# Kernel optimization log

Measured on AMD Instinct MI355X. Metric: run time of the kernel, lower is better.

The kernel has to match this reference:

```python
import jax, jax.numpy as jnp
import numpy as np

N = 100000      # nodes
E = 1600000     # edges (avg degree 16)
IN = 128
H = 128
OUT = 112
L = 4           # num GCN2Conv layers per net
NETS = 3        # ensemble size (hardcoded n=3 in module)
ALPHA = 0.1
THETA = 0.5


def setup_inputs() -> dict:
    key = jax.random.key(0)
    ks = jax.random.split(key, 9)
    x = jax.random.normal(ks[0], (N, IN), jnp.float32)
    edge_index = jax.random.randint(ks[1], (2, E), 0, N, dtype=jnp.int32).astype(jnp.int64)
    edge_weight = jax.random.uniform(ks[2], (E,), jnp.float32)
    # nn.Linear default init: U(-1/sqrt(fan_in), 1/sqrt(fan_in))
    s_in = 1.0 / np.sqrt(IN)
    s_h = 1.0 / np.sqrt(H)
    lin0_w = jax.random.uniform(ks[3], (NETS, IN, H), jnp.float32, -s_in, s_in)
    lin0_b = jax.random.uniform(ks[4], (NETS, H), jnp.float32, -s_in, s_in)
    lin1_w = jax.random.uniform(ks[5], (NETS, H, OUT), jnp.float32, -s_h, s_h)
    lin1_b = jax.random.uniform(ks[6], (NETS, OUT), jnp.float32, -s_h, s_h)
    # GCN2Conv shared weight per layer: glorot-ish uniform
    conv_w = jax.random.uniform(ks[7], (NETS, L, H, H), jnp.float32, -s_h, s_h)
    return {"x": x, "edge_index": edge_index, "edge_weight": edge_weight,
            "lin0_w": lin0_w, "lin0_b": lin0_b, "lin1_w": lin1_w,
            "lin1_b": lin1_b, "conv_w": conv_w}


def _net_forward(x, src, dst, ew, w0, b0, w1, b1, cw):
    # x: [N, IN] -> log-probs [N, OUT]; one GCN2 sub-net (eval mode, dropout=0)
    h = jax.nn.relu(x @ w0 + b0)           # [N, H]
    x0 = h
    for l in range(L):
        beta = float(np.log(THETA / (l + 1) + 1.0))
        # sparse propagation: adj_t @ h with 'add' aggregation
        agg = jax.ops.segment_sum(h[src] * ew[:, None], dst, num_segments=N)  # [N, H]
        t = (1.0 - ALPHA) * agg + ALPHA * x0        # initial residual
        h = jax.nn.relu((1.0 - beta) * t + beta * (t @ cw[l]))  # identity mapping
    out = h @ w1 + b1                       # [N, OUT]
    return jax.nn.log_softmax(out, axis=-1)


def reference(x, edge_index, edge_weight, lin0_w, lin0_b, lin1_w, lin1_b, conv_w):
    src, dst = edge_index[0], edge_index[1]
    outs = [
        _net_forward(x, src, dst, edge_weight,
                     lin0_w[n], lin0_b[n], lin1_w[n], lin1_b[n], conv_w[n])
        for n in range(NETS)
    ]
    return jnp.mean(jnp.stack(outs, axis=0), axis=0)  # [N, OUT]
```

## Files before the change

kernel.cpp:

```cpp
#include <hip/hip_runtime.h>
#include <hip/hip_bf16.h>

#define NNODES 100000
#define NEDGES 1600000
#define INF_   128
#define HF     128
#define OUTF   112
#define NLAYERS 4
#define NNETS  3

typedef __attribute__((ext_vector_type(8))) short bf16x8;
typedef __attribute__((ext_vector_type(8))) unsigned short u16x8;
typedef __attribute__((ext_vector_type(4))) float f32x4;
typedef __attribute__((ext_vector_type(2))) unsigned int u32x2;
typedef unsigned long long u64;
typedef unsigned int u32;

__device__ __forceinline__ float bf2f(short u){
  unsigned x = ((unsigned)(unsigned short)u) << 16;
  return __builtin_bit_cast(float, x);
}
__device__ __forceinline__ unsigned short f2bf(float f){
  unsigned u = __builtin_bit_cast(unsigned, f);
  u += 0x7fffu + ((u >> 16) & 1u);
  return (unsigned short)(u >> 16);
}
__device__ __forceinline__ float ub(u32 q, int j){ return (float)((q >> (8*j)) & 0xFF); }


__global__ void detect_fmt(const u64* __restrict__ ei64, int* __restrict__ flag){
  u64 v = ei64[threadIdx.x];
  u64 b = __ballot((v >> 32) != 0ull);
  if (threadIdx.x == 0) flag[0] = (b == 0ull) ? 1 : 0;
}

__device__ __forceinline__ int load_dst(const int* ei, int is64, int e){
  return is64 ? ei[2*(NEDGES + e)] : ei[NEDGES + e];
}
__device__ __forceinline__ int load_src(const int* ei, int is64, int e){
  return is64 ? ei[2*e] : ei[e];
}

__global__ void zero_counts(int* counts){
  int i = blockIdx.x*256 + threadIdx.x;
  if (i < NNODES) counts[i] = 0;
}

__global__ void hist_kernel(const int* __restrict__ ei, const int* __restrict__ flag, int* counts){
  int e = blockIdx.x*256 + threadIdx.x;
  if (e < NEDGES){
    int d = load_dst(ei, flag[0], e);
    if ((unsigned)d < NNODES) atomicAdd(&counts[d], 1);
  }
}

__global__ __launch_bounds__(256) void scan1(const int* __restrict__ counts,
                                             int* __restrict__ scanned,
                                             int* __restrict__ partials){
  __shared__ int s[256];
  int t = threadIdx.x, i = blockIdx.x*256 + t;
  int v = (i < NNODES) ? counts[i] : 0;
  s[t] = v; __syncthreads();
  for (int off=1; off<256; off<<=1){
    int a = (t >= off) ? s[t-off] : 0;
    __syncthreads();
    s[t] += a;
    __syncthreads();
  }
  if (i < NNODES) scanned[i] = s[t] - v;
  if (t == 255) partials[blockIdx.x] = s[255];
}

__global__ __launch_bounds__(512) void scan2(int* partials, int G){
  __shared__ int s[512];
  int t = threadIdx.x;
  int v = (t < G) ? partials[t] : 0;
  s[t] = v; __syncthreads();
  for (int off=1; off<512; off<<=1){
    int a = (t >= off) ? s[t-off] : 0;
    __syncthreads();
    s[t] += a;
    __syncthreads();
  }
  if (t < G) partials[t] = s[t] - v;
}

__global__ void scan3(const int* __restrict__ scanned, const int* __restrict__ partials,
                      int* __restrict__ row_ptr, int* __restrict__ cursor){
  int i = blockIdx.x*256 + threadIdx.x;
  if (i < NNODES){
    int v = scanned[i] + partials[i>>8];
    row_ptr[i] = v;
    cursor[i]  = v;
  } else if (i == NNODES){
    row_ptr[NNODES] = NEDGES;
  }
}

__global__ void scatter_kernel(const int* __restrict__ ei, const float* __restrict__ ew,
                               const int* __restrict__ flag,
                               int* cursor, u32* __restrict__ meta){
  int e = blockIdx.x*256 + threadIdx.x;
  if (e < NEDGES){
    int is64 = flag[0];
    int s = load_src(ei, is64, e);
    int d = load_dst(ei, is64, e);
    float w = __builtin_nontemporal_load(&ew[e]);
    if ((unsigned)d < NNODES && (unsigned)s < NNODES){
      int pos = atomicAdd(&cursor[d], 1);
      if ((unsigned)pos < NEDGES){
        u32 wb = __builtin_bit_cast(u32, w);
        u32 w15 = ((wb + 0x8000u) >> 16) & 0x7FFFu;
        __builtin_nontemporal_store((w15 << 17) | (u32)s, &meta[pos]);
      }
    }
  }
}

__global__ void prep_w(const float* __restrict__ w0, const float* __restrict__ cw,
                       const float* __restrict__ w1,
                       short* __restrict__ w0t, short* __restrict__ cwt, short* __restrict__ w1t){
  int i = blockIdx.x*256 + threadIdx.x;
  const int n0 = NNETS*HF*HF;
  const int n1 = NNETS*NLAYERS*HF*HF;
  const int n2 = NNETS*OUTF*HF;
  if (i < n0){
    int net = i/(HF*HF), r = i%(HF*HF), c = r/HF, k = r%HF;
    w0t[i] = (short)f2bf(w0[(size_t)net*HF*HF + k*HF + c]);
  } else if (i < n0 + n1){
    int j = i - n0;
    int nl = j/(HF*HF), r = j%(HF*HF), c = r/HF, kp = r%HF;
    int k = ((kp&7)<<4) | (kp>>3);
    cwt[j] = (short)f2bf(cw[(size_t)nl*HF*HF + k*HF + c]);
  } else if (i < n0 + n1 + n2){
    int j = i - n0 - n1;
    int net = j/(OUTF*HF), r = j%(OUTF*HF), c = r/HF, kp = r%HF;
    int k = ((kp&7)<<4) | (kp>>3);
    w1t[j] = (short)f2bf(w1[(size_t)net*HF*OUTF + k*OUTF + c]);
  }
}

__global__ __launch_bounds__(256) void gemm_in(
    const float* __restrict__ x, const short* __restrict__ w0t, const float* __restrict__ b0,
    unsigned char* __restrict__ h8, float* __restrict__ sc,
    unsigned char* __restrict__ x08, float* __restrict__ scx)
{
  __shared__ short As[128*128];
  const int t = threadIdx.x;
  const int rowBase = blockIdx.x * 128;
  #pragma unroll
  for (int it=0; it<8; ++it){
    int r = it*16 + (t>>4);
    int k = (t&15)*8;
    int gr = rowBase + r;
    bf16x8 v = {0,0,0,0,0,0,0,0};
    if (gr < NNODES){
      f32x4 f0 = __builtin_nontemporal_load((const f32x4*)&x[(size_t)gr*128 + k]);
      f32x4 f1 = __builtin_nontemporal_load((const f32x4*)&x[(size_t)gr*128 + k + 4]);
      v[0]=(short)f2bf(f0[0]); v[1]=(short)f2bf(f0[1]); v[2]=(short)f2bf(f0[2]); v[3]=(short)f2bf(f0[3]);
      v[4]=(short)f2bf(f1[0]); v[5]=(short)f2bf(f1[1]); v[6]=(short)f2bf(f1[2]); v[7]=(short)f2bf(f1[3]);
    }
    *(bf16x8*)&As[r*128 + (k ^ ((r&7)<<3))] = v;
  }
  __syncthreads();

  const int wid = t>>6, lane = t&63;
  const int l16 = lane&15, kg = lane>>4;
  for (int net=0; net<NNETS; ++net){
    const short* Wt = w0t + (size_t)net*HF*HF;
    f32x4 acc[2][8];
    #pragma unroll
    for (int mt=0; mt<2; ++mt)
      #pragma unroll
      for (int nt=0; nt<8; ++nt){ acc[mt][nt][0]=0.f; acc[mt][nt][1]=0.f; acc[mt][nt][2]=0.f; acc[mt][nt][3]=0.f; }
    #pragma unroll
    for (int ks=0; ks<4; ++ks){
      int k0 = ks*32 + kg*8;
      bf16x8 a0, a1;
      { int r = wid*32 + l16;      a0 = *(const bf16x8*)&As[r*128 + (k0 ^ ((r&7)<<3))]; }
      { int r = wid*32 + 16 + l16; a1 = *(const bf16x8*)&As[r*128 + (k0 ^ ((r&7)<<3))]; }
      #pragma unroll
      for (int nt=0; nt<8; ++nt){
        bf16x8 b = *(const bf16x8*)&Wt[(size_t)(nt*16 + l16)*128 + k0];
        acc[0][nt] = __builtin_amdgcn_mfma_f32_16x16x32_bf16(a0, b, acc[0][nt], 0, 0, 0);
        acc[1][nt] = __builtin_amdgcn_mfma_f32_16x16x32_bf16(a1, b, acc[1][nt], 0, 0, 0);
      }
    }
    #pragma unroll
    for (int mt=0; mt<2; ++mt){
      #pragma unroll
      for (int j=0; j<4; ++j){
        int row = rowBase + wid*32 + mt*16 + kg*4 + j;
        float v[8]; float mx = 0.f;
        #pragma unroll
        for (int nt=0; nt<8; ++nt){
          float f = fmaxf(acc[mt][nt][j] + b0[net*HF + nt*16 + l16], 0.f);
          v[nt] = f; mx = fmaxf(mx, f);
        }
        #pragma unroll
        for (int off=1; off<16; off<<=1) mx = fmaxf(mx, __shfl_xor(mx, off));
        if (row < NNODES){
          float inv = (mx > 0.f) ? 255.f/mx : 0.f;
          u32 d0=0, d1=0;
          #pragma unroll
          for (int nt=0; nt<4; ++nt) d0 |= ((u32)(v[nt]*inv + 0.5f)) << (8*nt);
          #pragma unroll
          for (int nt=0; nt<4; ++nt) d1 |= ((u32)(v[4+nt]*inv + 0.5f)) << (8*nt);
          u32x2 pk; pk[0]=d0; pk[1]=d1;
          size_t off8 = (size_t)row*384 + net*128 + l16*8;
          *(u32x2*)&h8 [off8] = pk;
          *(u32x2*)&x08[off8] = pk;
          if (l16 == 0){ float s = mx * (1.f/255.f); sc[row*4 + net] = s; scx[row*4 + net] = s; }
        }
      }
    }
  }
}

__global__ __launch_bounds__(256) void gemm_mid(
    const unsigned char* __restrict__ agg8, const float* __restrict__ sca,
    const unsigned char* __restrict__ x08,  const float* __restrict__ scx,
    const short* __restrict__ W, const float beta,
    unsigned char* __restrict__ h8, float* __restrict__ sc)
{
  __shared__ short As[128*128];
  const int t = threadIdx.x;
  const int net = blockIdx.y;
  const int rowBase = blockIdx.x * 128;
  const short* Wt = W + (size_t)net*NLAYERS*HF*HF;

  #pragma unroll
  for (int it=0; it<8; ++it){
    int r = it*16 + (t>>4);
    int k = (t&15)*8;
    int gr = rowBase + r;
    bf16x8 v = {0,0,0,0,0,0,0,0};
    if (gr < NNODES){
      size_t off8 = (size_t)gr*384 + net*128 + k;
      u32x2 da = *(const u32x2*)&agg8[off8];
      u32x2 dx = *(const u32x2*)&x08[off8];
      float sa = 0.9f * sca[gr*4 + net];
      float sx = 0.1f * scx[gr*4 + net];
      #pragma unroll
      for (int j=0; j<4; ++j) v[j]   = (short)f2bf(sa*ub(da[0],j) + sx*ub(dx[0],j));
      #pragma unroll
      for (int j=0; j<4; ++j) v[4+j] = (short)f2bf(sa*ub(da[1],j) + sx*ub(dx[1],j));
    }
    *(bf16x8*)&As[r*128 + (k ^ ((r&7)<<3))] = v;
  }
  __syncthreads();

  const int wid = t>>6, lane = t&63;
  const int l16 = lane&15, kg = lane>>4;
  f32x4 acc[2][8];
  #pragma unroll
  for (int mt=0; mt<2; ++mt)
    #pragma unroll
    for (int nt=0; nt<8; ++nt){ acc[mt][nt][0]=0.f; acc[mt][nt][1]=0.f; acc[mt][nt][2]=0.f; acc[mt][nt][3]=0.f; }

  #pragma unroll
  for (int ks=0; ks<4; ++ks){
    int k0 = ks*32 + kg*8;
    bf16x8 a0, a1;
    { int r = wid*32 + l16;      a0 = *(const bf16x8*)&As[r*128 + (k0 ^ ((r&7)<<3))]; }
    { int r = wid*32 + 16 + l16; a1 = *(const bf16x8*)&As[r*128 + (k0 ^ ((r&7)<<3))]; }
    #pragma unroll
    for (int nt=0; nt<8; ++nt){
      bf16x8 b = *(const bf16x8*)&Wt[(size_t)(nt*16 + l16)*128 + k0];
      acc[0][nt] = __builtin_amdgcn_mfma_f32_16x16x32_bf16(a0, b, acc[0][nt], 0, 0, 0);
      acc[1][nt] = __builtin_amdgcn_mfma_f32_16x16x32_bf16(a1, b, acc[1][nt], 0, 0, 0);
    }
  }

  #pragma unroll
  for (int mt=0; mt<2; ++mt){
    #pragma unroll
    for (int j=0; j<4; ++j){
      int rl  = wid*32 + mt*16 + kg*4 + j;
      int row = rowBase + rl;
      float v[8]; float mx = 0.f;
      #pragma unroll
      for (int nt=0; nt<8; ++nt){
        int p = l16*8 + nt;
        float av = bf2f(As[rl*128 + (p ^ ((rl&7)<<3))]);
        float f = fmaxf((1.f-beta)*av + beta*acc[mt][nt][j], 0.f);
        v[nt] = f; mx = fmaxf(mx, f);
      }
      #pragma unroll
      for (int off=1; off<16; off<<=1) mx = fmaxf(mx, __shfl_xor(mx, off));
      if (row < NNODES){
        float inv = (mx > 0.f) ? 255.f/mx : 0.f;
        u32 d0=0, d1=0;
        #pragma unroll
        for (int nt=0; nt<4; ++nt) d0 |= ((u32)(v[nt]*inv + 0.5f)) << (8*nt);
        #pragma unroll
        for (int nt=0; nt<4; ++nt) d1 |= ((u32)(v[4+nt]*inv + 0.5f)) << (8*nt);
        u32x2 pk; pk[0]=d0; pk[1]=d1;
        *(u32x2*)&h8[(size_t)row*384 + net*128 + l16*8] = pk;
        if (l16 == 0) sc[row*4 + net] = mx * (1.f/255.f);
      }
    }
  }
}

__global__ __launch_bounds__(256) void gemm_out(
    const unsigned char* __restrict__ h8, const float* __restrict__ sc,
    const short* __restrict__ w1t, const float* __restrict__ b1,
    float* __restrict__ out)
{
  __shared__ short As[128*128];
  const int t = threadIdx.x;
  const int rowBase = blockIdx.x * 128;
  const int wid = t>>6, lane = t&63;
  const int l16 = lane&15, kg = lane>>4;

  f32x4 sum[2][7];
  #pragma unroll
  for (int mt=0; mt<2; ++mt)
    #pragma unroll
    for (int nt=0; nt<7; ++nt){ sum[mt][nt][0]=0.f; sum[mt][nt][1]=0.f; sum[mt][nt][2]=0.f; sum[mt][nt][3]=0.f; }

  for (int net=0; net<NNETS; ++net){
    __syncthreads();
    #pragma unroll
    for (int it=0; it<8; ++it){
      int r = it*16 + (t>>4);
      int k = (t&15)*8;
      int gr = rowBase + r;
      bf16x8 v = {0,0,0,0,0,0,0,0};
      if (gr < NNODES){
        u32x2 d = *(const u32x2*)&h8[(size_t)gr*384 + net*128 + k];
        float s = sc[gr*4 + net];
        #pragma unroll
        for (int j=0; j<4; ++j) v[j]   = (short)f2bf(s * ub(d[0],j));
        #pragma unroll
        for (int j=0; j<4; ++j) v[4+j] = (short)f2bf(s * ub(d[1],j));
      }
      *(bf16x8*)&As[r*128 + (k ^ ((r&7)<<3))] = v;
    }
    __syncthreads();

    const short* Wt = w1t + (size_t)net*OUTF*HF;
    f32x4 acc[2][7];
    #pragma unroll
    for (int mt=0; mt<2; ++mt)
      #pragma unroll
      for (int nt=0; nt<7; ++nt){ acc[mt][nt][0]=0.f; acc[mt][nt][1]=0.f; acc[mt][nt][2]=0.f; acc[mt][nt][3]=0.f; }
    #pragma unroll
    for (int ks=0; ks<4; ++ks){
      int k0 = ks*32 + kg*8;
      bf16x8 a0, a1;
      { int r = wid*32 + l16;      a0 = *(const bf16x8*)&As[r*128 + (k0 ^ ((r&7)<<3))]; }
      { int r = wid*32 + 16 + l16; a1 = *(const bf16x8*)&As[r*128 + (k0 ^ ((r&7)<<3))]; }
      #pragma unroll
      for (int nt=0; nt<7; ++nt){
        bf16x8 b = *(const bf16x8*)&Wt[(size_t)(nt*16 + l16)*128 + k0];
        acc[0][nt] = __builtin_amdgcn_mfma_f32_16x16x32_bf16(a0, b, acc[0][nt], 0, 0, 0);
        acc[1][nt] = __builtin_amdgcn_mfma_f32_16x16x32_bf16(a1, b, acc[1][nt], 0, 0, 0);
      }
    }
    #pragma unroll
    for (int mt=0; mt<2; ++mt)
      #pragma unroll
      for (int nt=0; nt<7; ++nt){
        float b = b1[net*OUTF + nt*16 + l16];
        #pragma unroll
        for (int j=0; j<4; ++j) acc[mt][nt][j] += b;
      }
    #pragma unroll
    for (int mt=0; mt<2; ++mt){
      #pragma unroll
      for (int j=0; j<4; ++j){
        float m = -3.4e38f;
        #pragma unroll
        for (int nt=0; nt<7; ++nt) m = fmaxf(m, acc[mt][nt][j]);
        #pragma unroll
        for (int k=1; k<16; k<<=1) m = fmaxf(m, __shfl_xor(m, k));
        float e = 0.f;
        #pragma unroll
        for (int nt=0; nt<7; ++nt) e += expf(acc[mt][nt][j] - m);
        #pragma unroll
        for (int k=1; k<16; k<<=1) e += __shfl_xor(e, k);
        float lse = m + logf(e);
        #pragma unroll
        for (int nt=0; nt<7; ++nt) sum[mt][nt][j] += acc[mt][nt][j] - lse;
      }
    }
  }

  #pragma unroll
  for (int mt=0; mt<2; ++mt){
    #pragma unroll
    for (int nt=0; nt<7; ++nt){
      #pragma unroll
      for (int j=0; j<4; ++j){
        int row = rowBase + wid*32 + mt*16 + kg*4 + j;
        if (row < NNODES)
          __builtin_nontemporal_store(sum[mt][nt][j] * (1.f/3.f),
                                      &out[(size_t)row*OUTF + nt*16 + l16]);
      }
    }
  }
}

__global__ __launch_bounds__(256) void spmm3(
    const int* __restrict__ row_ptr, const u32* __restrict__ meta,
    const unsigned char* __restrict__ h8, const float* __restrict__ sc,
    unsigned char* __restrict__ agg8, float* __restrict__ sca)
{
  int node = blockIdx.x*4 + (threadIdx.x>>6);
  int lane = threadIdx.x & 63;
  int q    = lane >> 4;
  int l16  = lane & 15;
  int start = row_ptr[node], end = row_ptr[node+1];
  float acc[3][8] = {{0.f},{0.f},{0.f}};
  int e = start + q;
  for (; e + 4 < end; e += 8){
    u32 m0 = __builtin_nontemporal_load(&meta[e]);
    u32 m1 = __builtin_nontemporal_load(&meta[e+4]);
    u32 s0 = m0 & 0x1FFFFu, s1 = m1 & 0x1FFFFu;
    float w0 = __builtin_bit_cast(float, (m0 >> 17) << 16);
    float w1 = __builtin_bit_cast(float, (m1 >> 17) << 16);
    f32x4 c0 = *(const f32x4*)&sc[s0*4];
    f32x4 c1 = *(const f32x4*)&sc[s1*4];
    const u32* p0 = (const u32*)(h8 + (size_t)s0*384 + l16*8);
    const u32* p1 = (const u32*)(h8 + (size_t)s1*384 + l16*8);
    u32x2 a0 = *(const u32x2*)(p0);
    u32x2 a1 = *(const u32x2*)(p0+32);
    u32x2 a2 = *(const u32x2*)(p0+64);
    u32x2 b0 = *(const u32x2*)(p1);
    u32x2 b1 = *(const u32x2*)(p1+32);
    u32x2 b2 = *(const u32x2*)(p1+64);
    float ws00 = w0*c0[0], ws01 = w0*c0[1], ws02 = w0*c0[2];
    float ws10 = w1*c1[0], ws11 = w1*c1[1], ws12 = w1*c1[2];
    #pragma unroll
    for (int j=0;j<4;++j){
      acc[0][j]   += ws00*ub(a0[0],j) + ws10*ub(b0[0],j);
      acc[0][j+4] += ws00*ub(a0[1],j) + ws10*ub(b0[1],j);
      acc[1][j]   += ws01*ub(a1[0],j) + ws11*ub(b1[0],j);
      acc[1][j+4] += ws01*ub(a1[1],j) + ws11*ub(b1[1],j);
      acc[2][j]   += ws02*ub(a2[0],j) + ws12*ub(b2[0],j);
      acc[2][j+4] += ws02*ub(a2[1],j) + ws12*ub(b2[1],j);
    }
  }
  for (; e < end; e += 4){
    u32 m0 = __builtin_nontemporal_load(&meta[e]);
    u32 s0 = m0 & 0x1FFFFu;
    float w0 = __builtin_bit_cast(float, (m0 >> 17) << 16);
    f32x4 c0 = *(const f32x4*)&sc[s0*4];
    const u32* p0 = (const u32*)(h8 + (size_t)s0*384 + l16*8);
    u32x2 a0 = *(const u32x2*)(p0);
    u32x2 a1 = *(const u32x2*)(p0+32);
    u32x2 a2 = *(const u32x2*)(p0+64);
    float ws00 = w0*c0[0], ws01 = w0*c0[1], ws02 = w0*c0[2];
    #pragma unroll
    for (int j=0;j<4;++j){
      acc[0][j]   += ws00*ub(a0[0],j);
      acc[0][j+4] += ws00*ub(a0[1],j);
      acc[1][j]   += ws01*ub(a1[0],j);
      acc[1][j+4] += ws01*ub(a1[1],j);
      acc[2][j]   += ws02*ub(a2[0],j);
      acc[2][j+4] += ws02*ub(a2[1],j);
    }
  }
  #pragma unroll
  for (int n=0;n<3;++n)
    #pragma unroll
    for (int j=0;j<8;++j){
      acc[n][j] += __shfl_xor(acc[n][j], 16);
      acc[n][j] += __shfl_xor(acc[n][j], 32);
    }
  if (q < 3){
    float mx = 0.f;
    #pragma unroll
    for (int j=0;j<8;++j) mx = fmaxf(mx, acc[q][j]);
    #pragma unroll
    for (int off=1; off<16; off<<=1) mx = fmaxf(mx, __shfl_xor(mx, off));
    float inv = (mx > 0.f) ? 255.f/mx : 0.f;
    u32 d0=0, d1=0;
    #pragma unroll
    for (int j=0;j<4;++j) d0 |= ((u32)(acc[q][j]*inv + 0.5f)) << (8*j);
    #pragma unroll
    for (int j=0;j<4;++j) d1 |= ((u32)(acc[q][4+j]*inv + 0.5f)) << (8*j);
    u32x2 pk; pk[0]=d0; pk[1]=d1;
    *(u32x2*)&agg8[(size_t)node*384 + q*128 + l16*8] = pk;
    if (l16 == 0) sca[node*4 + q] = mx * (1.f/255.f);
  }
}

extern "C" void kernel_launch(void* const* d_in, const int* in_sizes, int n_in,
                              void* d_out, int out_size, void* d_ws, size_t ws_size,
                              hipStream_t stream){
  const float* x  = (const float*)d_in[0];
  const int*   ei = (const int*)d_in[1];
  const float* ew = (const float*)d_in[2];
  const float* w0 = (const float*)d_in[3];
  const float* b0 = (const float*)d_in[4];
  const float* w1 = (const float*)d_in[5];
  const float* b1 = (const float*)d_in[6];
  const float* cw = (const float*)d_in[7];
  float* out = (float*)d_out;

  char* ws = (char*)d_ws;
  size_t o = 0;
  auto alloc = [&](size_t b){ size_t r = o; o += (b + 255) & ~(size_t)255; return r; };
  int*   flag     = (int*)(ws + alloc(256));
  int*   counts   = (int*)(ws + alloc((size_t)NNODES*4));
  int*   scanned  = (int*)(ws + alloc((size_t)NNODES*4));
  int*   cursor   = (int*)(ws + alloc((size_t)NNODES*4));
  int*   row_ptr  = (int*)(ws + alloc((size_t)(NNODES+1)*4));
  int*   partials = (int*)(ws + alloc(512*4));
  u32*   meta     = (u32*)(ws + alloc((size_t)NEDGES*4));
  short* w0t = (short*)(ws + alloc((size_t)NNETS*HF*HF*2));
  short* cwt = (short*)(ws + alloc((size_t)NNETS*NLAYERS*HF*HF*2));
  short* w1t = (short*)(ws + alloc((size_t)NNETS*OUTF*HF*2));
  unsigned char* h8   = (unsigned char*)(ws + alloc((size_t)NNODES*NNETS*128));
  float* sc  = (float*)(ws + alloc((size_t)NNODES*4*4));
  unsigned char* x08  = (unsigned char*)(ws + alloc((size_t)NNODES*NNETS*128));
  float* scx = (float*)(ws + alloc((size_t)NNODES*4*4));
  unsigned char* agg8 = (unsigned char*)(ws + alloc((size_t)NNODES*NNETS*128));
  float* sca = (float*)(ws + alloc((size_t)NNODES*4*4));
  (void)ws_size; (void)in_sizes; (void)n_in; (void)out_size;

  detect_fmt    <<<1,   64,  0, stream>>>((const u64*)ei, flag);
  zero_counts   <<<391, 256, 0, stream>>>(counts);
  hist_kernel   <<<6250,256, 0, stream>>>(ei, flag, counts);
  scan1         <<<391, 256, 0, stream>>>(counts, scanned, partials);
  scan2         <<<1,   512, 0, stream>>>(partials, 391);
  scan3         <<<391, 256, 0, stream>>>(scanned, partials, row_ptr, cursor);
  scatter_kernel<<<6250,256, 0, stream>>>(ei, ew, flag, cursor, meta);

  prep_w<<<1128, 256, 0, stream>>>(w0, cw, w1, w0t, cwt, w1t);

  gemm_in<<<782, 256, 0, stream>>>(x, w0t, b0, h8, sc, x08, scx);
  for (int l=0; l<NLAYERS; ++l){
    float beta = logf(0.5f/(float)(l+1) + 1.0f);
    spmm3<<<25000, 256, 0, stream>>>(row_ptr, meta, h8, sc, agg8, sca);
    gemm_mid<<<dim3(782,3), 256, 0, stream>>>(agg8, sca, x08, scx,
                                              cwt + (size_t)l*HF*HF, beta, h8, sc);
  }
  gemm_out<<<782, 256, 0, stream>>>(h8, sc, w1t, b1, out);
}
```

Baseline: 1.249 ms.

## Use grid-stride persistent SpMM and rank-based CSR scatter without second atomic pass

The SpMM kernel becomes a persistent grid-stride loop over nodes with a fixed block count, where it previously launched one wave per node. It also computes 32-bit byte offsets with shifts instead of 64-bit multiplies. CSR construction now records each edge's atomic rank during the histogram, so the scatter computes its position without a second atomic pass and the zero kernel becomes a memset. The cost is an extra 6.4MB rank buffer, and the fixed-stride node assignment can leave waves unevenly loaded.

```diff
diff --git a/kernel.cpp b/kernel.cpp
--- a/kernel.cpp
+++ b/kernel.cpp
@@ -8,10 +8,13 @@
 #define OUTF   112
 #define NLAYERS 4
 #define NNETS  3
+#define SPMM_BLOCKS 2048
+#define SPMM_WAVES  (SPMM_BLOCKS*4)
 
 typedef __attribute__((ext_vector_type(8))) short bf16x8;
 typedef __attribute__((ext_vector_type(8))) unsigned short u16x8;
 typedef __attribute__((ext_vector_type(4))) float f32x4;
+typedef __attribute__((ext_vector_type(2))) float f32x2;
 typedef __attribute__((ext_vector_type(2))) unsigned int u32x2;
 typedef unsigned long long u64;
 typedef unsigned int u32;
@@ -41,16 +44,12 @@
   return is64 ? ei[2*e] : ei[e];
 }
 
-__global__ void zero_counts(int* counts){
-  int i = blockIdx.x*256 + threadIdx.x;
-  if (i < NNODES) counts[i] = 0;
-}
-
-__global__ void hist_kernel(const int* __restrict__ ei, const int* __restrict__ flag, int* counts){
+__global__ void hist_kernel(const int* __restrict__ ei, const int* __restrict__ flag,
+                            int* counts, int* __restrict__ rank){
   int e = blockIdx.x*256 + threadIdx.x;
   if (e < NEDGES){
     int d = load_dst(ei, flag[0], e);
-    if ((unsigned)d < NNODES) atomicAdd(&counts[d], 1);
+    if ((unsigned)d < NNODES) rank[e] = atomicAdd(&counts[d], 1);
   }
 }
 
@@ -86,12 +85,10 @@
 }
 
 __global__ void scan3(const int* __restrict__ scanned, const int* __restrict__ partials,
-                      int* __restrict__ row_ptr, int* __restrict__ cursor){
+                      int* __restrict__ row_ptr){
   int i = blockIdx.x*256 + threadIdx.x;
   if (i < NNODES){
-    int v = scanned[i] + partials[i>>8];
-    row_ptr[i] = v;
-    cursor[i]  = v;
+    row_ptr[i] = scanned[i] + partials[i>>8];
   } else if (i == NNODES){
     row_ptr[NNODES] = NEDGES;
   }
@@ -99,7 +96,8 @@
 
 __global__ void scatter_kernel(const int* __restrict__ ei, const float* __restrict__ ew,
                                const int* __restrict__ flag,
-                               int* cursor, u32* __restrict__ meta){
+                               const int* __restrict__ row_ptr, const int* __restrict__ rank,
+                               u32* __restrict__ meta){
   int e = blockIdx.x*256 + threadIdx.x;
   if (e < NEDGES){
     int is64 = flag[0];
@@ -107,7 +105,7 @@
     int d = load_dst(ei, is64, e);
     float w = __builtin_nontemporal_load(&ew[e]);
     if ((unsigned)d < NNODES && (unsigned)s < NNODES){
-      int pos = atomicAdd(&cursor[d], 1);
+      int pos = row_ptr[d] + rank[e];
       if ((unsigned)pos < NEDGES){
         u32 wb = __builtin_bit_cast(u32, w);
         u32 w15 = ((wb + 0x8000u) >> 16) & 0x7FFFu;
@@ -408,83 +406,87 @@
     const unsigned char* __restrict__ h8, const float* __restrict__ sc,
     unsigned char* __restrict__ agg8, float* __restrict__ sca)
 {
-  int node = blockIdx.x*4 + (threadIdx.x>>6);
-  int lane = threadIdx.x & 63;
-  int q    = lane >> 4;
-  int l16  = lane & 15;
-  int start = row_ptr[node], end = row_ptr[node+1];
-  float acc[3][8] = {{0.f},{0.f},{0.f}};
-  int e = start + q;
-  for (; e + 4 < end; e += 8){
-    u32 m0 = __builtin_nontemporal_load(&meta[e]);
-    u32 m1 = __builtin_nontemporal_load(&meta[e+4]);
-    u32 s0 = m0 & 0x1FFFFu, s1 = m1 & 0x1FFFFu;
-    float w0 = __builtin_bit_cast(float, (m0 >> 17) << 16);
-    float w1 = __builtin_bit_cast(float, (m1 >> 17) << 16);
-    f32x4 c0 = *(const f32x4*)&sc[s0*4];
-    f32x4 c1 = *(const f32x4*)&sc[s1*4];
-    const u32* p0 = (const u32*)(h8 + (size_t)s0*384 + l16*8);
-    const u32* p1 = (const u32*)(h8 + (size_t)s1*384 + l16*8);
-    u32x2 a0 = *(const u32x2*)(p0);
-    u32x2 a1 = *(const u32x2*)(p0+32);
-    u32x2 a2 = *(const u32x2*)(p0+64);
-    u32x2 b0 = *(const u32x2*)(p1);
-    u32x2 b1 = *(const u32x2*)(p1+32);
-    u32x2 b2 = *(const u32x2*)(p1+64);
-    float ws00 = w0*c0[0], ws01 = w0*c0[1], ws02 = w0*c0[2];
-    float ws10 = w1*c1[0], ws11 = w1*c1[1], ws12 = w1*c1[2];
-    #pragma unroll
-    for (int j=0;j<4;++j){
-      acc[0][j]   += ws00*ub(a0[0],j) + ws10*ub(b0[0],j);
-      acc[0][j+4] += ws00*ub(a0[1],j) + ws10*ub(b0[1],j);
-      acc[1][j]   += ws01*ub(a1[0],j) + ws11*ub(b1[0],j);
-      acc[1][j+4] += ws01*ub(a1[1],j) + ws11*ub(b1[1],j);
-      acc[2][j]   += ws02*ub(a2[0],j) + ws12*ub(b2[0],j);
-      acc[2][j+4] += ws02*ub(a2[1],j) + ws12*ub(b2[1],j);
-    }
-  }
-  for (; e < end; e += 4){
-    u32 m0 = __builtin_nontemporal_load(&meta[e]);
-    u32 s0 = m0 & 0x1FFFFu;
-    float w0 = __builtin_bit_cast(float, (m0 >> 17) << 16);
-    f32x4 c0 = *(const f32x4*)&sc[s0*4];
-    const u32* p0 = (const u32*)(h8 + (size_t)s0*384 + l16*8);
-    u32x2 a0 = *(const u32x2*)(p0);
-    u32x2 a1 = *(const u32x2*)(p0+32);
-    u32x2 a2 = *(const u32x2*)(p0+64);
-    float ws00 = w0*c0[0], ws01 = w0*c0[1], ws02 = w0*c0[2];
-    #pragma unroll
-    for (int j=0;j<4;++j){
-      acc[0][j]   += ws00*ub(a0[0],j);
-      acc[0][j+4] += ws00*ub(a0[1],j);
-      acc[1][j]   += ws01*ub(a1[0],j);
-      acc[1][j+4] += ws01*ub(a1[1],j);
-      acc[2][j]   += ws02*ub(a2[0],j);
-      acc[2][j+4] += ws02*ub(a2[1],j);
-    }
-  }
-  #pragma unroll
-  for (int n=0;n<3;++n)
-    #pragma unroll
-    for (int j=0;j<8;++j){
-      acc[n][j] += __shfl_xor(acc[n][j], 16);
-      acc[n][j] += __shfl_xor(acc[n][j], 32);
-    }
-  if (q < 3){
-    float mx = 0.f;
-    #pragma unroll
-    for (int j=0;j<8;++j) mx = fmaxf(mx, acc[q][j]);
-    #pragma unroll
-    for (int off=1; off<16; off<<=1) mx = fmaxf(mx, __shfl_xor(mx, off));
-    float inv = (mx > 0.f) ? 255.f/mx : 0.f;
-    u32 d0=0, d1=0;
-    #pragma unroll
-    for (int j=0;j<4;++j) d0 |= ((u32)(acc[q][j]*inv + 0.5f)) << (8*j);
-    #pragma unroll
-    for (int j=0;j<4;++j) d1 |= ((u32)(acc[q][4+j]*inv + 0.5f)) << (8*j);
-    u32x2 pk; pk[0]=d0; pk[1]=d1;
-    *(u32x2*)&agg8[(size_t)node*384 + q*128 + l16*8] = pk;
-    if (l16 == 0) sca[node*4 + q] = mx * (1.f/255.f);
+  const int wgid = blockIdx.x*4 + (threadIdx.x>>6);
+  const int lane = threadIdx.x & 63;
+  const int q    = lane >> 4;
+  const int l16  = lane & 15;
+  const u32 base_l = (u32)l16*8;
+
+  for (int node = wgid; node < NNODES; node += SPMM_WAVES){
+    int start = row_ptr[node], end = row_ptr[node+1];
+    float acc[3][8] = {{0.f},{0.f},{0.f}};
+    int e = start + q;
+    for (; e + 4 < end; e += 8){
+      u32 m0 = __builtin_nontemporal_load(&meta[e]);
+      u32 m1 = __builtin_nontemporal_load(&meta[e+4]);
+      u32 s0 = m0 & 0x1FFFFu, s1 = m1 & 0x1FFFFu;
+      u32 o0 = (s0<<8) + (s0<<7) + base_l;
+      u32 o1 = (s1<<8) + (s1<<7) + base_l;
+      float w0 = __builtin_bit_cast(float, (m0 >> 17) << 16);
+      float w1 = __builtin_bit_cast(float, (m1 >> 17) << 16);
+      f32x4 c0 = *(const f32x4*)&sc[s0*4];
+      f32x4 c1 = *(const f32x4*)&sc[s1*4];
+      u32x2 a0 = *(const u32x2*)(h8 + o0);
+      u32x2 a1 = *(const u32x2*)(h8 + o0 + 128);
+      u32x2 a2 = *(const u32x2*)(h8 + o0 + 256);
+      u32x2 b0 = *(const u32x2*)(h8 + o1);
+      u32x2 b1 = *(const u32x2*)(h8 + o1 + 128);
+      u32x2 b2 = *(const u32x2*)(h8 + o1 + 256);
+      float ws00 = w0*c0[0], ws01 = w0*c0[1], ws02 = w0*c0[2];
+      float ws10 = w1*c1[0], ws11 = w1*c1[1], ws12 = w1*c1[2];
+      #pragma unroll
+      for (int j=0;j<4;++j){
+        acc[0][j]   += ws00*ub(a0[0],j) + ws10*ub(b0[0],j);
+        acc[0][j+4] += ws00*ub(a0[1],j) + ws10*ub(b0[1],j);
+        acc[1][j]   += ws01*ub(a1[0],j) + ws11*ub(b1[0],j);
+        acc[1][j+4] += ws01*ub(a1[1],j) + ws11*ub(b1[1],j);
+        acc[2][j]   += ws02*ub(a2[0],j) + ws12*ub(b2[0],j);
+        acc[2][j+4] += ws02*ub(a2[1],j) + ws12*ub(b2[1],j);
+      }
+    }
+    for (; e < end; e += 4){
+      u32 m0 = __builtin_nontemporal_load(&meta[e]);
+      u32 s0 = m0 & 0x1FFFFu;
+      u32 o0 = (s0<<8) + (s0<<7) + base_l;
+      float w0 = __builtin_bit_cast(float, (m0 >> 17) << 16);
+      f32x4 c0 = *(const f32x4*)&sc[s0*4];
+      u32x2 a0 = *(const u32x2*)(h8 + o0);
+      u32x2 a1 = *(const u32x2*)(h8 + o0 + 128);
+      u32x2 a2 = *(const u32x2*)(h8 + o0 + 256);
+      float ws00 = w0*c0[0], ws01 = w0*c0[1], ws02 = w0*c0[2];
+      #pragma unroll
+      for (int j=0;j<4;++j){
+        acc[0][j]   += ws00*ub(a0[0],j);
+        acc[0][j+4] += ws00*ub(a0[1],j);
+        acc[1][j]   += ws01*ub(a1[0],j);
+        acc[1][j+4] += ws01*ub(a1[1],j);
+        acc[2][j]   += ws02*ub(a2[0],j);
+        acc[2][j+4] += ws02*ub(a2[1],j);
+      }
+    }
+    #pragma unroll
+    for (int n=0;n<3;++n)
+      #pragma unroll
+      for (int j=0;j<8;++j){
+        acc[n][j] += __shfl_xor(acc[n][j], 16);
+        acc[n][j] += __shfl_xor(acc[n][j], 32);
+      }
+    if (q < 3){
+      float mx = 0.f;
+      #pragma unroll
+      for (int j=0;j<8;++j) mx = fmaxf(mx, acc[q][j]);
+      #pragma unroll
+      for (int off=1; off<16; off<<=1) mx = fmaxf(mx, __shfl_xor(mx, off));
+      float inv = (mx > 0.f) ? 255.f/mx : 0.f;
+      u32 d0=0, d1=0;
+      #pragma unroll
+      for (int j=0;j<4;++j) d0 |= ((u32)(acc[q][j]*inv + 0.5f)) << (8*j);
+      #pragma unroll
+      for (int j=0;j<4;++j) d1 |= ((u32)(acc[q][4+j]*inv + 0.5f)) << (8*j);
+      u32x2 pk; pk[0]=d0; pk[1]=d1;
+      *(u32x2*)&agg8[(size_t)node*384 + q*128 + base_l] = pk;
+      if (l16 == 0) sca[node*4 + q] = mx * (1.f/255.f);
+    }
   }
 }
 
@@ -507,9 +509,9 @@
   int*   flag     = (int*)(ws + alloc(256));
   int*   counts   = (int*)(ws + alloc((size_t)NNODES*4));
   int*   scanned  = (int*)(ws + alloc((size_t)NNODES*4));
-  int*   cursor   = (int*)(ws + alloc((size_t)NNODES*4));
   int*   row_ptr  = (int*)(ws + alloc((size_t)(NNODES+1)*4));
   int*   partials = (int*)(ws + alloc(512*4));
+  int*   rank     = (int*)(ws + alloc((size_t)NEDGES*4));
   u32*   meta     = (u32*)(ws + alloc((size_t)NEDGES*4));
   short* w0t = (short*)(ws + alloc((size_t)NNETS*HF*HF*2));
   short* cwt = (short*)(ws + alloc((size_t)NNETS*NLAYERS*HF*HF*2));
@@ -522,20 +524,20 @@
   float* sca = (float*)(ws + alloc((size_t)NNODES*4*4));
   (void)ws_size; (void)in_sizes; (void)n_in; (void)out_size;
 
+  hipMemsetAsync(counts, 0, (size_t)NNODES*4, stream);
   detect_fmt    <<<1,   64,  0, stream>>>((const u64*)ei, flag);
-  zero_counts   <<<391, 256, 0, stream>>>(counts);
-  hist_kernel   <<<6250,256, 0, stream>>>(ei, flag, counts);
+  hist_kernel   <<<6250,256, 0, stream>>>(ei, flag, counts, rank);
   scan1         <<<391, 256, 0, stream>>>(counts, scanned, partials);
   scan2         <<<1,   512, 0, stream>>>(partials, 391);
-  scan3         <<<391, 256, 0, stream>>>(scanned, partials, row_ptr, cursor);
-  scatter_kernel<<<6250,256, 0, stream>>>(ei, ew, flag, cursor, meta);
+  scan3         <<<391, 256, 0, stream>>>(scanned, partials, row_ptr);
+  scatter_kernel<<<6250,256, 0, stream>>>(ei, ew, flag, row_ptr, rank, meta);
 
   prep_w<<<1128, 256, 0, stream>>>(w0, cw, w1, w0t, cwt, w1t);
 
   gemm_in<<<782, 256, 0, stream>>>(x, w0t, b0, h8, sc, x08, scx);
   for (int l=0; l<NLAYERS; ++l){
     float beta = logf(0.5f/(float)(l+1) + 1.0f);
-    spmm3<<<25000, 256, 0, stream>>>(row_ptr, meta, h8, sc, agg8, sca);
+    spmm3<<<SPMM_BLOCKS, 256, 0, stream>>>(row_ptr, meta, h8, sc, agg8, sca);
     gemm_mid<<<dim3(782,3), 256, 0, stream>>>(agg8, sca, x08, scx,
                                               cwt + (size_t)l*HF*HF, beta, h8, sc);
   }
```

Measured after the change: 1.307 ms. 1.05x slower.
